# Kernel tuning notes

Hardware: AMD Instinct MI355X
Metric: run time of the kernel (lower is better)

The kernel has to match this reference:

```python
import jax, jax.numpy as jnp
import numpy as np

N = 4096
D = 256
THRESH = 0.04  # default threshold arg of MultiLayerGCN.forward


def setup_inputs() -> dict:
    key = jax.random.key(0)
    ks = jax.random.split(key, 6)
    A = jax.random.normal(ks[0], (N, N), dtype=jnp.float32)
    features = jax.random.normal(ks[1], (N, D), dtype=jnp.float32)
    s = 0.02
    W1 = jax.random.normal(ks[2], (D, D), dtype=jnp.float32) * s
    b1 = jax.random.normal(ks[3], (D,), dtype=jnp.float32) * s
    W2 = jax.random.normal(ks[4], (D, D), dtype=jnp.float32) * s
    b2 = jax.random.normal(ks[5], (D,), dtype=jnp.float32) * s
    return {"A": A, "features": features, "W1": W1, "b1": b1, "W2": W2, "b2": b2}


def _graph_conv(C, out_isqrt, in_isqrt, h, W, b):
    # DGL GraphConv, norm='both': scale src by out_deg^-1/2, aggregate over
    # edges u->v (rst[v] = sum_u C[u,v] * h[u]), scale dst by in_deg^-1/2.
    h = (h * out_isqrt[:, None]) @ W            # [N, out]
    agg = jnp.einsum('uv,ud->vd', C, h)          # C^T @ h, honoring edge direction
    return agg * in_isqrt[:, None] + b


def reference(A, features, W1, b1, W2, b2):
    dt = features.dtype
    mask = (A >= THRESH).astype(dt)
    # add_edges(nodes, nodes) adds self loops on top of surviving diagonal -> counts
    C = mask + jnp.eye(A.shape[0], dtype=dt)
    out_deg = jnp.maximum(C.sum(axis=1), 1.0)    # clamp(min=1) as in DGL
    in_deg = jnp.maximum(C.sum(axis=0), 1.0)
    out_isqrt = jax.lax.rsqrt(out_deg)
    in_isqrt = jax.lax.rsqrt(in_deg)
    h1 = jax.nn.relu(_graph_conv(C, out_isqrt, in_isqrt, features, W1, b1))
    h2 = jax.nn.relu(_graph_conv(C, out_isqrt, in_isqrt, h1, W2, b2))
    return (h1, h2)
```

## Files before the change

kernel.cpp:

```cpp
#include <hip/hip_runtime.h>
#include <stdint.h>

#define NN 4096
#define DD 256
#define TH 0.04f

typedef __attribute__((ext_vector_type(4))) float f32x4;
typedef __attribute__((ext_vector_type(16))) float f32x16;
typedef __attribute__((ext_vector_type(8))) short s16x8;
typedef unsigned short us;

__device__ __forceinline__ us f2bf(float f) {
  union { float f; uint32_t u; } x; x.f = f;
  uint32_t u = x.u;
  return (us)((u + 0x7FFFu + ((u >> 16) & 1u)) >> 16);
}
__device__ __forceinline__ float bf2f(us h) {
  union { uint32_t u; float f; } x; x.u = ((uint32_t)h) << 16;
  return x.f;
}

__device__ __forceinline__ void hw_selfstage(const float* __restrict__ H,
                                             const float* __restrict__ W,
                                             int u0,
                                             us* __restrict__ hWb,
                                             us* __restrict__ hWbP,
                                             char* smem) {
  us (*hs)[264] = reinterpret_cast<us(*)[264]>(smem);
  us (*wt)[34]  = reinterpret_cast<us(*)[34]>(smem + 16 * 264 * 2);
  us (*lt)[260] = reinterpret_cast<us(*)[260]>(smem + 16 * 264 * 2 + 256 * 34 * 2);
  const int t = threadIdx.x;
#pragma unroll
  for (int rep = 0; rep < 4; ++rep) {
    const int flat = rep * 256 + t;
    const int row = flat >> 6, c4 = (flat & 63) * 4;
    f32x4 v = *reinterpret_cast<const f32x4*>(H + (size_t)(u0 + row) * DD + c4);
    uint2 pw;
    pw.x = (uint32_t)f2bf(v[0]) | ((uint32_t)f2bf(v[1]) << 16);
    pw.y = (uint32_t)f2bf(v[2]) | ((uint32_t)f2bf(v[3]) << 16);
    *reinterpret_cast<uint2*>(&hs[row][c4]) = pw;
  }
  const int lane = t & 63, w = t >> 6, l15 = lane & 15, l4 = lane >> 4;
  const f32x4 z = {0.f, 0.f, 0.f, 0.f};
  f32x4 acc[4];
#pragma unroll
  for (int jn = 0; jn < 4; ++jn) acc[jn] = z;
#pragma unroll 1
  for (int ks = 0; ks < 8; ++ks) {
    __syncthreads();
#pragma unroll
    for (int rr = 0; rr < 8; ++rr) {
      const int flat = rr * 256 + t;
      const int k = flat >> 6, d0 = (flat & 63) * 4;
      f32x4 wv = *reinterpret_cast<const f32x4*>(W + (size_t)(ks * 32 + k) * DD + d0);
      wt[d0 + 0][k] = f2bf(wv[0]);
      wt[d0 + 1][k] = f2bf(wv[1]);
      wt[d0 + 2][k] = f2bf(wv[2]);
      wt[d0 + 3][k] = f2bf(wv[3]);
    }
    __syncthreads();
    s16x8 af = *reinterpret_cast<const s16x8*>(&hs[l15][ks * 32 + l4 * 8]);
#pragma unroll
    for (int jn = 0; jn < 4; ++jn) {
      const int dt = w * 4 + jn;
      s16x8 bf = *reinterpret_cast<const s16x8*>(&wt[dt * 16 + l15][l4 * 8]);
      acc[jn] = __builtin_amdgcn_mfma_f32_16x16x32_bf16(af, bf, acc[jn], 0, 0, 0);
    }
  }
#pragma unroll
  for (int jn = 0; jn < 4; ++jn) {
    const int d = w * 64 + jn * 16 + l15;
#pragma unroll
    for (int r = 0; r < 4; ++r) {
      const int ul = l4 * 4 + r;
      us hv = f2bf(acc[jn][r]);
      hWb[(size_t)(u0 + ul) * DD + d] = hv;
      lt[ul][d] = hv;
    }
  }
  __syncthreads();
  const int sg = u0 >> 4;
#pragma unroll
  for (int cc = 0; cc < 2; ++cc) {
    const int c = t * 2 + cc;
    const int dt = c >> 6, lc = c & 63;
    const int ub = (lc >> 5) * 8;
    const int d = dt * 32 + (lc & 31);
    uint4 val;
    val.x = (uint32_t)lt[ub + 0][d] | ((uint32_t)lt[ub + 1][d] << 16);
    val.y = (uint32_t)lt[ub + 2][d] | ((uint32_t)lt[ub + 3][d] << 16);
    val.z = (uint32_t)lt[ub + 4][d] | ((uint32_t)lt[ub + 5][d] << 16);
    val.w = (uint32_t)lt[ub + 6][d] | ((uint32_t)lt[ub + 7][d] << 16);
    *reinterpret_cast<uint4*>(hWbP + ((size_t)dt * 256 + sg) * 512 + lc * 8) = val;
  }
}

__global__ __launch_bounds__(256) void k_scanhw1(const float* __restrict__ A,
                                                 const float* __restrict__ feat,
                                                 const float* __restrict__ W1,
                                                 const float* __restrict__ W2,
                                                 us* __restrict__ bitsT,
                                                 unsigned char* __restrict__ colpart,
                                                 float* __restrict__ oif,
                                                 us* __restrict__ oib,
                                                 us* __restrict__ hWb1,
                                                 us* __restrict__ hWbP1,
                                                 us* __restrict__ W2TbP) {
  __shared__ __align__(16) char smem[34176];
  const int b = blockIdx.x, t = threadIdx.x;
  const int r3 = b % 3;
  if (r3 == 2) {
    hw_selfstage(feat, W1, (b / 3) * 16, hWb1, hWbP1, smem);
    return;
  }
  const int sb = (b / 3) * 2 + r3;
  us* lds16 = reinterpret_cast<us*>(smem);
  const int u0 = sb * 8;
  uint32_t cs[16];
#pragma unroll
  for (int k = 0; k < 16; ++k) cs[k] = 0;
#pragma unroll
  for (int rb = 0; rb < 2; ++rb) {
    f32x4 a[4][4];
#pragma unroll
    for (int r = 0; r < 4; ++r) {
      const f32x4* p = reinterpret_cast<const f32x4*>(A + (size_t)(u0 + rb * 4 + r) * NN + t * 16);
#pragma unroll
      for (int c = 0; c < 4; ++c) a[r][c] = p[c];
    }
#pragma unroll
    for (int r = 0; r < 4; ++r) {
      uint32_t m = 0;
#pragma unroll
      for (int c = 0; c < 4; ++c)
#pragma unroll
        for (int j = 0; j < 4; ++j) m |= (a[r][c][j] >= TH ? 1u : 0u) << (c * 4 + j);
      lds16[t * 8 + rb * 4 + r] = (us)m;
#pragma unroll
      for (int k = 0; k < 16; ++k) cs[k] += (m >> k) & 1u;
    }
  }
  uint4 pk;
  pk.x = cs[0]  | (cs[1]  << 8) | (cs[2]  << 16) | (cs[3]  << 24);
  pk.y = cs[4]  | (cs[5]  << 8) | (cs[6]  << 16) | (cs[7]  << 24);
  pk.z = cs[8]  | (cs[9]  << 8) | (cs[10] << 16) | (cs[11] << 24);
  pk.w = cs[12] | (cs[13] << 8) | (cs[14] << 16) | (cs[15] << 24);
  *reinterpret_cast<uint4*>(colpart + (size_t)sb * 4096 + t * 16) = pk;
  __syncthreads();
  uint4 wv4 = *reinterpret_cast<const uint4*>(&lds16[t * 8]);
  *reinterpret_cast<uint4*>(bitsT + (size_t)t * 4096 + u0) = wv4;
  if (t < 64) {
    const int r = t >> 3, part = t & 7;
    uint32_t s = 0;
#pragma unroll
    for (int wv = part * 32; wv < part * 32 + 32; ++wv)
      s += (uint32_t)__popc((uint32_t)lds16[wv * 8 + r]);
    s += __shfl_down(s, 4, 8);
    s += __shfl_down(s, 2, 8);
    s += __shfl_down(s, 1, 8);
    if (part == 0) {
      float val = rsqrtf((float)(s + 1u));
      oif[u0 + r] = val;
      oib[u0 + r] = f2bf(val);
    }
  }
  if (sb < 16) {
    const int base = sb * 4096 + t * 16;
#pragma unroll
    for (int e = 0; e < 16; ++e) {
      const int idx = base + e;
      const int frag = idx >> 9, pos = idx & 511;
      const int lc = pos >> 3, j = pos & 7;
      const int dt = frag >> 3, ks = frag & 7;
      const int k = ks * 32 + (lc >> 4) * 8 + j;
      const int d = dt * 16 + (lc & 15);
      W2TbP[idx] = f2bf(W2[k * 256 + d]);
    }
  }
}

__global__ __launch_bounds__(256) void k_hw2(const float* __restrict__ H,
                                             const us* __restrict__ WP,
                                             const float* __restrict__ oif,
                                             us* __restrict__ hWb,
                                             us* __restrict__ hWbP) {
  __shared__ us hs[16][264];
  __shared__ us lt[16][260];
  const int t = threadIdx.x;
  const int u0 = blockIdx.x * 16;
#pragma unroll
  for (int rep = 0; rep < 4; ++rep) {
    const int flat = rep * 256 + t;
    const int row = flat >> 6, c4 = (flat & 63) * 4;
    f32x4 v = *reinterpret_cast<const f32x4*>(H + (size_t)(u0 + row) * DD + c4);
    uint2 pw;
    pw.x = (uint32_t)f2bf(v[0]) | ((uint32_t)f2bf(v[1]) << 16);
    pw.y = (uint32_t)f2bf(v[2]) | ((uint32_t)f2bf(v[3]) << 16);
    *reinterpret_cast<uint2*>(&hs[row][c4]) = pw;
  }
  __syncthreads();
  const int lane = t & 63, w = t >> 6, l15 = lane & 15, l4 = lane >> 4;
  const f32x4 z = {0.f, 0.f, 0.f, 0.f};
  f32x4 acc[4];
#pragma unroll
  for (int jn = 0; jn < 4; ++jn) acc[jn] = z;
#pragma unroll
  for (int ks = 0; ks < 8; ++ks) {
    s16x8 af = *reinterpret_cast<const s16x8*>(&hs[l15][ks * 32 + l4 * 8]);
#pragma unroll
    for (int jn = 0; jn < 4; ++jn) {
      const int dt = w * 4 + jn;
      s16x8 bf = *reinterpret_cast<const s16x8*>(WP + ((size_t)dt * 8 + ks) * 512 + lane * 8);
      acc[jn] = __builtin_amdgcn_mfma_f32_16x16x32_bf16(af, bf, acc[jn], 0, 0, 0);
    }
  }
  float oifv[4];
#pragma unroll
  for (int r = 0; r < 4; ++r) oifv[r] = oif[u0 + l4 * 4 + r];
#pragma unroll
  for (int jn = 0; jn < 4; ++jn) {
    const int d = w * 64 + jn * 16 + l15;
#pragma unroll
    for (int r = 0; r < 4; ++r) {
      const int ul = l4 * 4 + r;
      us hv = f2bf(acc[jn][r] * oifv[r]);
      hWb[(size_t)(u0 + ul) * DD + d] = hv;
      lt[ul][d] = hv;
    }
  }
  __syncthreads();
  const int sg = u0 >> 4;
#pragma unroll
  for (int cc = 0; cc < 2; ++cc) {
    const int c = t * 2 + cc;
    const int dt = c >> 6, lc = c & 63;
    const int ub = (lc >> 5) * 8;
    const int d = dt * 32 + (lc & 31);
    uint4 val;
    val.x = (uint32_t)lt[ub + 0][d] | ((uint32_t)lt[ub + 1][d] << 16);
    val.y = (uint32_t)lt[ub + 2][d] | ((uint32_t)lt[ub + 3][d] << 16);
    val.z = (uint32_t)lt[ub + 4][d] | ((uint32_t)lt[ub + 5][d] << 16);
    val.w = (uint32_t)lt[ub + 6][d] | ((uint32_t)lt[ub + 7][d] << 16);
    *reinterpret_cast<uint4*>(hWbP + ((size_t)dt * 256 + sg) * 512 + lc * 8) = val;
  }
}

template <int L1>
__global__ __launch_bounds__(512, 2) void k_spmm(const us* __restrict__ bitsT,
                                                 const us* __restrict__ hWbP,
                                                 const us* __restrict__ hWb,
                                                 const float* __restrict__ oif,
                                                 const us* __restrict__ oib,
                                                 const unsigned char* __restrict__ colpart,
                                                 float* __restrict__ ii_g,
                                                 const float* __restrict__ bias,
                                                 float* __restrict__ dst) {
  __shared__ float lds[4 * 64 * 68];
  __shared__ float ii_s[64];
  const int t = threadIdx.x, bq = blockIdx.x;
  const int lane = t & 63, w = t >> 6;
  const int mi = w & 1, kc = w >> 1;
  const int xcd = bq & 7, jj = bq >> 3;
  const int vt = xcd * 8 + (jj >> 2), dq = jj & 3;
  const int V0 = vt * 64, D0 = dq * 64;

  const int l31 = lane & 31, l5 = lane >> 5;
  const uint32_t sh = lane & 15;
  const int wvl = vt * 4 + mi * 2 + ((lane >> 4) & 1);
  const us* Ab = bitsT + (size_t)wvl * 4096 + kc * 1024 + l5 * 8;
  const us* Ob = oib + kc * 1024 + l5 * 8;
  const us* Bp0 = hWbP + ((size_t)(dq * 2 + 0) * 256 + kc * 64) * 512 + lane * 8;
  const us* Bp1 = hWbP + ((size_t)(dq * 2 + 1) * 256 + kc * 64) * 512 + lane * 8;

  f32x16 acc0, acc1;
#pragma unroll
  for (int q = 0; q < 16; ++q) { acc0[q] = 0.f; acc1[q] = 0.f; }

  uint4 h[4]; s16x8 o[4], p0[4], p1[4];
#pragma unroll
  for (int sl = 0; sl < 4; ++sl) {
    h[sl]  = *reinterpret_cast<const uint4*>(Ab + sl * 16);
    if (L1) o[sl] = *reinterpret_cast<const s16x8*>(Ob + sl * 16);
    p0[sl] = *reinterpret_cast<const s16x8*>(Bp0 + (size_t)sl * 512);
    p1[sl] = *reinterpret_cast<const s16x8*>(Bp1 + (size_t)sl * 512);
  }

#pragma unroll 1
  for (int it = 0; it < 16; ++it) {
#pragma unroll
    for (int sl = 0; sl < 4; ++sl) {
      union { s16x8 v; uint32_t u[4]; } af;
      uint32_t m;
      if (L1) {
        const uint32_t* ou = reinterpret_cast<const uint32_t*>(&o[sl]);
        m = (h[sl].x >> sh) & 0x10001u; af.u[0] = ou[0] & ((m << 16) - m);
        m = (h[sl].y >> sh) & 0x10001u; af.u[1] = ou[1] & ((m << 16) - m);
        m = (h[sl].z >> sh) & 0x10001u; af.u[2] = ou[2] & ((m << 16) - m);
        m = (h[sl].w >> sh) & 0x10001u; af.u[3] = ou[3] & ((m << 16) - m);
      } else {
        m = (h[sl].x >> sh) & 0x10001u; af.u[0] = m * 0x3F80u;
        m = (h[sl].y >> sh) & 0x10001u; af.u[1] = m * 0x3F80u;
        m = (h[sl].z >> sh) & 0x10001u; af.u[2] = m * 0x3F80u;
        m = (h[sl].w >> sh) & 0x10001u; af.u[3] = m * 0x3F80u;
      }
      acc0 = __builtin_amdgcn_mfma_f32_32x32x16_bf16(af.v, p0[sl], acc0, 0, 0, 0);
      acc1 = __builtin_amdgcn_mfma_f32_32x32x16_bf16(af.v, p1[sl], acc1, 0, 0, 0);
      const int ns = (it * 4 + sl + 4) & 63;
      h[sl]  = *reinterpret_cast<const uint4*>(Ab + ns * 16);
      if (L1) o[sl] = *reinterpret_cast<const s16x8*>(Ob + ns * 16);
      p0[sl] = *reinterpret_cast<const s16x8*>(Bp0 + (size_t)ns * 512);
      p1[sl] = *reinterpret_cast<const s16x8*>(Bp1 + (size_t)ns * 512);
    }
  }

  if (L1) {
    uint32_t* sc = reinterpret_cast<uint32_t*>(lds);
    const int v4 = t & 15, c = t >> 4;
    uint32_t s0 = 0, s1 = 0;
#pragma unroll 4
    for (int r = 0; r < 16; ++r) {
      uint32_t x = *reinterpret_cast<const uint32_t*>(colpart + (size_t)(c * 16 + r) * 4096 + V0 + v4 * 4);
      s0 += x & 0x00FF00FFu;
      s1 += (x >> 8) & 0x00FF00FFu;
    }
    sc[(c * 16 + v4) * 2] = s0;
    sc[(c * 16 + v4) * 2 + 1] = s1;
    __syncthreads();
    if (t < 64) {
      const int v4b = t >> 2, sub = t & 3;
      const int reg = sub & 1, hi = sub >> 1;
      uint32_t s = 0;
#pragma unroll
      for (int cc = 0; cc < 32; ++cc)
        s += (sc[(cc * 16 + v4b) * 2 + reg] >> (hi * 16)) & 0xFFFFu;
      float val = rsqrtf((float)(s + 1u));
      ii_s[t] = val;
      ii_g[V0 + t] = val;
    }
    __syncthreads();
  } else {
    if (t < 64) ii_s[t] = ii_g[V0 + t];
  }

  float* buf = lds + (size_t)kc * (64 * 68);
#pragma unroll
  for (int reg = 0; reg < 16; ++reg) {
    const int row = (reg & 3) + 8 * (reg >> 2) + 4 * l5;
    buf[(mi * 32 + row) * 68 + l31] = acc0[reg];
    buf[(mi * 32 + row) * 68 + 32 + l31] = acc1[reg];
  }
  __syncthreads();

  const int vloc = t >> 3, d8 = (t & 7) * 8;
  const int v = V0 + vloc;
  const float* base = lds + vloc * 68 + d8;
  f32x4 s0v = *reinterpret_cast<const f32x4*>(base);
  f32x4 s1v = *reinterpret_cast<const f32x4*>(base + 4);
#pragma unroll
  for (int q = 1; q < 4; ++q) {
    s0v += *reinterpret_cast<const f32x4*>(base + q * (64 * 68));
    s1v += *reinterpret_cast<const f32x4*>(base + q * (64 * 68) + 4);
  }
  union { s16x8 v; us u[8]; } self;
  self.v = *reinterpret_cast<const s16x8*>(hWb + (size_t)v * DD + D0 + d8);
  const float iv = ii_s[vloc];
  const float ov = L1 ? oif[v] : 1.0f;
  const f32x4 bi0 = *reinterpret_cast<const f32x4*>(bias + D0 + d8);
  const f32x4 bi1 = *reinterpret_cast<const f32x4*>(bias + D0 + d8 + 4);
  f32x4 o0, o1;
#pragma unroll
  for (int e = 0; e < 4; ++e) {
    o0[e] = fmaxf((s0v[e] + ov * bf2f(self.u[e])) * iv + bi0[e], 0.f);
    o1[e] = fmaxf((s1v[e] + ov * bf2f(self.u[e + 4])) * iv + bi1[e], 0.f);
  }
  f32x4* po = reinterpret_cast<f32x4*>(dst + (size_t)v * DD + D0 + d8);
  po[0] = o0; po[1] = o1;
}

extern "C" void kernel_launch(void* const* d_in, const int* in_sizes, int n_in,
                              void* d_out, int out_size, void* d_ws, size_t ws_size,
                              hipStream_t stream) {
  const float* A    = (const float*)d_in[0];
  const float* feat = (const float*)d_in[1];
  const float* W1   = (const float*)d_in[2];
  const float* b1   = (const float*)d_in[3];
  const float* W2   = (const float*)d_in[4];
  const float* b2   = (const float*)d_in[5];
  float* out = (float*)d_out;
  char* ws = (char*)d_ws;

  us*            bitsT   = (us*)ws;
  unsigned char* colpart = (unsigned char*)(ws + (2u << 20));
  us*            hWbP1   = (us*)(ws + (4u << 20));
  us*            hWb1    = (us*)(ws + (6u << 20));
  us*            hWbP2   = (us*)(ws + (8u << 20));
  us*            hWb2    = (us*)(ws + (10u << 20));
  us*            W2TbP   = (us*)(ws + (12u << 20));
  float*         oif     = (float*)(ws + (12u << 20) + (1u << 17));
  us*            oib     = (us*)(ws + (12u << 20) + (1u << 17) + (16u << 10));
  float*         ii_g    = (float*)(ws + (12u << 20) + (1u << 17) + (24u << 10));

  k_scanhw1<<<768, 256, 0, stream>>>(A, feat, W1, W2, bitsT, colpart, oif, oib,
                                     hWb1, hWbP1, W2TbP);
  k_spmm<1><<<256, 512, 0, stream>>>(bitsT, hWbP1, hWb1, oif, oib, colpart,
                                     ii_g, b1, out);
  k_hw2<<<256, 256, 0, stream>>>(out, W2TbP, oif, hWb2, hWbP2);
  k_spmm<0><<<256, 512, 0, stream>>>(bitsT, hWbP2, hWb2, oif, oib, colpart,
                                     ii_g, b2, out + (size_t)NN * DD);
}
```

Measured before the change: 70.94 us.

## Fuse layer-1 aggregation with layer-2 feature transform into one kernel

Replaces the layer-1 SpMM plus separate hW2 GEMM kernel with a single kernel in which each block owns 16 destination rows across all 256 feature columns. It aggregates with 16x16x32 MFMAs, computes in-degree norms, applies bias/ReLU, then immediately multiplies by W2 from LDS to emit the layer-2 packed operands. It also folds the out-degree scaling into the layer-2 operand so the second SpMM drops the oif multiply. The hWbP1 packing layout changes to suit the new kernel. This removes one launch and a global round trip of h1, but each block now streams the full bit matrix row and the whole K range with smaller MFMA tiles, which may reduce reuse of the B operand.

```diff
diff --git a/kernel.cpp b/kernel.cpp
--- a/kernel.cpp
+++ b/kernel.cpp
@@ -79,19 +79,20 @@
     }
   }
   __syncthreads();
-  const int sg = u0 >> 4;
-#pragma unroll
-  for (int cc = 0; cc < 2; ++cc) {
-    const int c = t * 2 + cc;
-    const int dt = c >> 6, lc = c & 63;
-    const int ub = (lc >> 5) * 8;
-    const int d = dt * 32 + (lc & 31);
+  const int ks2 = u0 >> 5, half = (u0 >> 4) & 1;
+#pragma unroll
+  for (int e = 0; e < 2; ++e) {
+    const int s = t * 2 + e;
+    const int f = s >> 5, lrel = s & 31;
+    const int l = half * 32 + lrel;
+    const int ub = (lrel >> 4) * 8;
+    const int d = f * 16 + (lrel & 15);
     uint4 val;
     val.x = (uint32_t)lt[ub + 0][d] | ((uint32_t)lt[ub + 1][d] << 16);
     val.y = (uint32_t)lt[ub + 2][d] | ((uint32_t)lt[ub + 3][d] << 16);
     val.z = (uint32_t)lt[ub + 4][d] | ((uint32_t)lt[ub + 5][d] << 16);
     val.w = (uint32_t)lt[ub + 6][d] | ((uint32_t)lt[ub + 7][d] << 16);
-    *reinterpret_cast<uint4*>(hWbP + ((size_t)dt * 256 + sg) * 512 + lc * 8) = val;
+    *reinterpret_cast<uint4*>(hWbP + ((size_t)f * 128 + ks2) * 512 + l * 8) = val;
   }
 }
 
@@ -179,82 +180,155 @@
   }
 }
 
-__global__ __launch_bounds__(256) void k_hw2(const float* __restrict__ H,
-                                             const us* __restrict__ WP,
-                                             const float* __restrict__ oif,
-                                             us* __restrict__ hWb,
-                                             us* __restrict__ hWbP) {
-  __shared__ us hs[16][264];
-  __shared__ us lt[16][260];
-  const int t = threadIdx.x;
-  const int u0 = blockIdx.x * 16;
-#pragma unroll
-  for (int rep = 0; rep < 4; ++rep) {
-    const int flat = rep * 256 + t;
-    const int row = flat >> 6, c4 = (flat & 63) * 4;
-    f32x4 v = *reinterpret_cast<const f32x4*>(H + (size_t)(u0 + row) * DD + c4);
-    uint2 pw;
-    pw.x = (uint32_t)f2bf(v[0]) | ((uint32_t)f2bf(v[1]) << 16);
-    pw.y = (uint32_t)f2bf(v[2]) | ((uint32_t)f2bf(v[3]) << 16);
-    *reinterpret_cast<uint2*>(&hs[row][c4]) = pw;
-  }
-  __syncthreads();
-  const int lane = t & 63, w = t >> 6, l15 = lane & 15, l4 = lane >> 4;
-  const f32x4 z = {0.f, 0.f, 0.f, 0.f};
-  f32x4 acc[4];
-#pragma unroll
-  for (int jn = 0; jn < 4; ++jn) acc[jn] = z;
+__global__ __launch_bounds__(512, 2) void k_l1f(const us* __restrict__ bitsT,
+                                                const us* __restrict__ hWbP1,
+                                                const us* __restrict__ hWb1,
+                                                const float* __restrict__ oif,
+                                                const us* __restrict__ oib,
+                                                const unsigned char* __restrict__ colpart,
+                                                const us* __restrict__ W2TbP,
+                                                float* __restrict__ ii_g,
+                                                const float* __restrict__ b1,
+                                                float* __restrict__ out,
+                                                us* __restrict__ hWb2,
+                                                us* __restrict__ hWbP2) {
+  __shared__ __align__(16) uint32_t sc[128 * 4 * 2];
+  __shared__ us g[16][264];
+  __shared__ us p2l[16][264];
+  __shared__ float ii_s[16];
+  const int t = threadIdx.x, wv = blockIdx.x;
+  const int lane = t & 63, w = t >> 6;
+  const int V0 = wv * 16;
+  const int l15 = lane & 15, l4 = lane >> 4;
+  const uint32_t sh = (uint32_t)l15;
+
+  const us* Ab = bitsT + (size_t)wv * 4096 + l4 * 8;
+  const us* Ob = oib + l4 * 8;
+  const us* Bp0 = hWbP1 + ((size_t)(w * 2 + 0) * 128) * 512 + lane * 8;
+  const us* Bp1 = hWbP1 + ((size_t)(w * 2 + 1) * 128) * 512 + lane * 8;
+
+  f32x4 acc0 = {0.f, 0.f, 0.f, 0.f}, acc1 = {0.f, 0.f, 0.f, 0.f};
+  uint4 h[4]; s16x8 o[4], p0[4], p1[4];
+#pragma unroll
+  for (int sl = 0; sl < 4; ++sl) {
+    h[sl]  = *reinterpret_cast<const uint4*>(Ab + sl * 32);
+    o[sl]  = *reinterpret_cast<const s16x8*>(Ob + sl * 32);
+    p0[sl] = *reinterpret_cast<const s16x8*>(Bp0 + (size_t)sl * 512);
+    p1[sl] = *reinterpret_cast<const s16x8*>(Bp1 + (size_t)sl * 512);
+  }
+#pragma unroll 1
+  for (int it = 0; it < 32; ++it) {
+#pragma unroll
+    for (int sl = 0; sl < 4; ++sl) {
+      union { s16x8 v; uint32_t u[4]; } af;
+      const uint32_t* ou = reinterpret_cast<const uint32_t*>(&o[sl]);
+      uint32_t m;
+      m = (h[sl].x >> sh) & 0x10001u; af.u[0] = ou[0] & ((m << 16) - m);
+      m = (h[sl].y >> sh) & 0x10001u; af.u[1] = ou[1] & ((m << 16) - m);
+      m = (h[sl].z >> sh) & 0x10001u; af.u[2] = ou[2] & ((m << 16) - m);
+      m = (h[sl].w >> sh) & 0x10001u; af.u[3] = ou[3] & ((m << 16) - m);
+      acc0 = __builtin_amdgcn_mfma_f32_16x16x32_bf16(af.v, p0[sl], acc0, 0, 0, 0);
+      acc1 = __builtin_amdgcn_mfma_f32_16x16x32_bf16(af.v, p1[sl], acc1, 0, 0, 0);
+      const int ns = (it * 4 + sl + 4) & 127;
+      h[sl]  = *reinterpret_cast<const uint4*>(Ab + ns * 32);
+      o[sl]  = *reinterpret_cast<const s16x8*>(Ob + ns * 32);
+      p0[sl] = *reinterpret_cast<const s16x8*>(Bp0 + (size_t)ns * 512);
+      p1[sl] = *reinterpret_cast<const s16x8*>(Bp1 + (size_t)ns * 512);
+    }
+  }
+
+  {
+    const int v4 = t & 3, c = t >> 2;
+    uint32_t s0 = 0, s1 = 0;
+#pragma unroll
+    for (int r = 0; r < 4; ++r) {
+      uint32_t x = *reinterpret_cast<const uint32_t*>(colpart + (size_t)(c * 4 + r) * 4096 + V0 + v4 * 4);
+      s0 += x & 0x00FF00FFu;
+      s1 += (x >> 8) & 0x00FF00FFu;
+    }
+    sc[(c * 4 + v4) * 2] = s0;
+    sc[(c * 4 + v4) * 2 + 1] = s1;
+  }
+  __syncthreads();
+  if (t < 16) {
+    const int v4b = t >> 2, sub = t & 3;
+    const int reg = sub & 1, hi = sub >> 1;
+    uint32_t s = 0;
+#pragma unroll 8
+    for (int c2 = 0; c2 < 128; ++c2)
+      s += (sc[(c2 * 4 + v4b) * 2 + reg] >> (hi * 16)) & 0xFFFFu;
+    float val = rsqrtf((float)(s + 1u));
+    ii_s[t] = val;
+    ii_g[V0 + t] = val;
+  }
+  __syncthreads();
+
+  {
+    const int d0 = w * 32 + l15, d1 = d0 + 16;
+    const float bv0 = b1[d0], bv1 = b1[d1];
+#pragma unroll
+    for (int r = 0; r < 4; ++r) {
+      const int vloc = l4 * 4 + r;
+      const int v = V0 + vloc;
+      const float iv = ii_s[vloc];
+      const float ov = oif[v];
+      const float self0 = bf2f(hWb1[(size_t)v * DD + d0]);
+      const float self1 = bf2f(hWb1[(size_t)v * DD + d1]);
+      const float h10 = fmaxf((acc0[r] + ov * self0) * iv + bv0, 0.f);
+      const float h11 = fmaxf((acc1[r] + ov * self1) * iv + bv1, 0.f);
+      out[(size_t)v * DD + d0] = h10;
+      out[(size_t)v * DD + d1] = h11;
+      g[vloc][d0] = f2bf(h10 * ov);
+      g[vloc][d1] = f2bf(h11 * ov);
+    }
+  }
+  __syncthreads();
+
+  f32x4 q0 = {0.f, 0.f, 0.f, 0.f}, q1 = {0.f, 0.f, 0.f, 0.f};
 #pragma unroll
   for (int ks = 0; ks < 8; ++ks) {
-    s16x8 af = *reinterpret_cast<const s16x8*>(&hs[l15][ks * 32 + l4 * 8]);
-#pragma unroll
-    for (int jn = 0; jn < 4; ++jn) {
-      const int dt = w * 4 + jn;
-      s16x8 bf = *reinterpret_cast<const s16x8*>(WP + ((size_t)dt * 8 + ks) * 512 + lane * 8);
-      acc[jn] = __builtin_amdgcn_mfma_f32_16x16x32_bf16(af, bf, acc[jn], 0, 0, 0);
-    }
-  }
-  float oifv[4];
-#pragma unroll
-  for (int r = 0; r < 4; ++r) oifv[r] = oif[u0 + l4 * 4 + r];
-#pragma unroll
-  for (int jn = 0; jn < 4; ++jn) {
-    const int d = w * 64 + jn * 16 + l15;
-#pragma unroll
-    for (int r = 0; r < 4; ++r) {
-      const int ul = l4 * 4 + r;
-      us hv = f2bf(acc[jn][r] * oifv[r]);
-      hWb[(size_t)(u0 + ul) * DD + d] = hv;
-      lt[ul][d] = hv;
-    }
-  }
-  __syncthreads();
-  const int sg = u0 >> 4;
-#pragma unroll
-  for (int cc = 0; cc < 2; ++cc) {
-    const int c = t * 2 + cc;
-    const int dt = c >> 6, lc = c & 63;
+    s16x8 af = *reinterpret_cast<const s16x8*>(&g[l15][ks * 32 + l4 * 8]);
+    s16x8 w0 = *reinterpret_cast<const s16x8*>(W2TbP + ((size_t)(w * 2 + 0) * 8 + ks) * 512 + lane * 8);
+    s16x8 w1 = *reinterpret_cast<const s16x8*>(W2TbP + ((size_t)(w * 2 + 1) * 8 + ks) * 512 + lane * 8);
+    q0 = __builtin_amdgcn_mfma_f32_16x16x32_bf16(af, w0, q0, 0, 0, 0);
+    q1 = __builtin_amdgcn_mfma_f32_16x16x32_bf16(af, w1, q1, 0, 0, 0);
+  }
+#pragma unroll
+  for (int r = 0; r < 4; ++r) {
+    const int vloc = l4 * 4 + r;
+    p2l[vloc][w * 32 + l15] = f2bf(q0[r]);
+    p2l[vloc][w * 32 + 16 + l15] = f2bf(q1[r]);
+  }
+  __syncthreads();
+
+  {
+    const int row = t >> 5, d8 = (t & 31) * 8;
+    uint4 val;
+    val.x = (uint32_t)p2l[row][d8 + 0] | ((uint32_t)p2l[row][d8 + 1] << 16);
+    val.y = (uint32_t)p2l[row][d8 + 2] | ((uint32_t)p2l[row][d8 + 3] << 16);
+    val.z = (uint32_t)p2l[row][d8 + 4] | ((uint32_t)p2l[row][d8 + 5] << 16);
+    val.w = (uint32_t)p2l[row][d8 + 6] | ((uint32_t)p2l[row][d8 + 7] << 16);
+    *reinterpret_cast<uint4*>(hWb2 + (size_t)(V0 + row) * DD + d8) = val;
+  }
+  {
+    const int f = t >> 6, lc = t & 63;
     const int ub = (lc >> 5) * 8;
-    const int d = dt * 32 + (lc & 31);
+    const int d = f * 32 + (lc & 31);
     uint4 val;
-    val.x = (uint32_t)lt[ub + 0][d] | ((uint32_t)lt[ub + 1][d] << 16);
-    val.y = (uint32_t)lt[ub + 2][d] | ((uint32_t)lt[ub + 3][d] << 16);
-    val.z = (uint32_t)lt[ub + 4][d] | ((uint32_t)lt[ub + 5][d] << 16);
-    val.w = (uint32_t)lt[ub + 6][d] | ((uint32_t)lt[ub + 7][d] << 16);
-    *reinterpret_cast<uint4*>(hWbP + ((size_t)dt * 256 + sg) * 512 + lc * 8) = val;
-  }
-}
-
-template <int L1>
-__global__ __launch_bounds__(512, 2) void k_spmm(const us* __restrict__ bitsT,
-                                                 const us* __restrict__ hWbP,
-                                                 const us* __restrict__ hWb,
-                                                 const float* __restrict__ oif,
-                                                 const us* __restrict__ oib,
-                                                 const unsigned char* __restrict__ colpart,
-                                                 float* __restrict__ ii_g,
-                                                 const float* __restrict__ bias,
-                                                 float* __restrict__ dst) {
+    val.x = (uint32_t)p2l[ub + 0][d] | ((uint32_t)p2l[ub + 1][d] << 16);
+    val.y = (uint32_t)p2l[ub + 2][d] | ((uint32_t)p2l[ub + 3][d] << 16);
+    val.z = (uint32_t)p2l[ub + 4][d] | ((uint32_t)p2l[ub + 5][d] << 16);
+    val.w = (uint32_t)p2l[ub + 6][d] | ((uint32_t)p2l[ub + 7][d] << 16);
+    *reinterpret_cast<uint4*>(hWbP2 + ((size_t)f * 256 + wv) * 512 + lc * 8) = val;
+  }
+}
+
+__global__ __launch_bounds__(512, 2) void k_spmm2(const us* __restrict__ bitsT,
+                                                  const us* __restrict__ hWbP,
+                                                  const us* __restrict__ hWb,
+                                                  const float* __restrict__ ii_g,
+                                                  const float* __restrict__ bias,
+                                                  float* __restrict__ dst) {
   __shared__ float lds[4 * 64 * 68];
   __shared__ float ii_s[64];
   const int t = threadIdx.x, bq = blockIdx.x;
@@ -268,7 +342,6 @@
   const uint32_t sh = lane & 15;
   const int wvl = vt * 4 + mi * 2 + ((lane >> 4) & 1);
   const us* Ab = bitsT + (size_t)wvl * 4096 + kc * 1024 + l5 * 8;
-  const us* Ob = oib + kc * 1024 + l5 * 8;
   const us* Bp0 = hWbP + ((size_t)(dq * 2 + 0) * 256 + kc * 64) * 512 + lane * 8;
   const us* Bp1 = hWbP + ((size_t)(dq * 2 + 1) * 256 + kc * 64) * 512 + lane * 8;
 
@@ -276,11 +349,10 @@
 #pragma unroll
   for (int q = 0; q < 16; ++q) { acc0[q] = 0.f; acc1[q] = 0.f; }
 
-  uint4 h[4]; s16x8 o[4], p0[4], p1[4];
+  uint4 h[4]; s16x8 p0[4], p1[4];
 #pragma unroll
   for (int sl = 0; sl < 4; ++sl) {
     h[sl]  = *reinterpret_cast<const uint4*>(Ab + sl * 16);
-    if (L1) o[sl] = *reinterpret_cast<const s16x8*>(Ob + sl * 16);
     p0[sl] = *reinterpret_cast<const s16x8*>(Bp0 + (size_t)sl * 512);
     p1[sl] = *reinterpret_cast<const s16x8*>(Bp1 + (size_t)sl * 512);
   }
@@ -291,56 +363,20 @@
     for (int sl = 0; sl < 4; ++sl) {
       union { s16x8 v; uint32_t u[4]; } af;
       uint32_t m;
-      if (L1) {
-        const uint32_t* ou = reinterpret_cast<const uint32_t*>(&o[sl]);
-        m = (h[sl].x >> sh) & 0x10001u; af.u[0] = ou[0] & ((m << 16) - m);
-        m = (h[sl].y >> sh) & 0x10001u; af.u[1] = ou[1] & ((m << 16) - m);
-        m = (h[sl].z >> sh) & 0x10001u; af.u[2] = ou[2] & ((m << 16) - m);
-        m = (h[sl].w >> sh) & 0x10001u; af.u[3] = ou[3] & ((m << 16) - m);
-      } else {
-        m = (h[sl].x >> sh) & 0x10001u; af.u[0] = m * 0x3F80u;
-        m = (h[sl].y >> sh) & 0x10001u; af.u[1] = m * 0x3F80u;
-        m = (h[sl].z >> sh) & 0x10001u; af.u[2] = m * 0x3F80u;
-        m = (h[sl].w >> sh) & 0x10001u; af.u[3] = m * 0x3F80u;
-      }
+      m = (h[sl].x >> sh) & 0x10001u; af.u[0] = m * 0x3F80u;
+      m = (h[sl].y >> sh) & 0x10001u; af.u[1] = m * 0x3F80u;
+      m = (h[sl].z >> sh) & 0x10001u; af.u[2] = m * 0x3F80u;
+      m = (h[sl].w >> sh) & 0x10001u; af.u[3] = m * 0x3F80u;
       acc0 = __builtin_amdgcn_mfma_f32_32x32x16_bf16(af.v, p0[sl], acc0, 0, 0, 0);
       acc1 = __builtin_amdgcn_mfma_f32_32x32x16_bf16(af.v, p1[sl], acc1, 0, 0, 0);
       const int ns = (it * 4 + sl + 4) & 63;
       h[sl]  = *reinterpret_cast<const uint4*>(Ab + ns * 16);
-      if (L1) o[sl] = *reinterpret_cast<const s16x8*>(Ob + ns * 16);
       p0[sl] = *reinterpret_cast<const s16x8*>(Bp0 + (size_t)ns * 512);
       p1[sl] = *reinterpret_cast<const s16x8*>(Bp1 + (size_t)ns * 512);
     }
   }
 
-  if (L1) {
-    uint32_t* sc = reinterpret_cast<uint32_t*>(lds);
-    const int v4 = t & 15, c = t >> 4;
-    uint32_t s0 = 0, s1 = 0;
-#pragma unroll 4
-    for (int r = 0; r < 16; ++r) {
-      uint32_t x = *reinterpret_cast<const uint32_t*>(colpart + (size_t)(c * 16 + r) * 4096 + V0 + v4 * 4);
-      s0 += x & 0x00FF00FFu;
-      s1 += (x >> 8) & 0x00FF00FFu;
-    }
-    sc[(c * 16 + v4) * 2] = s0;
-    sc[(c * 16 + v4) * 2 + 1] = s1;
-    __syncthreads();
-    if (t < 64) {
-      const int v4b = t >> 2, sub = t & 3;
-      const int reg = sub & 1, hi = sub >> 1;
-      uint32_t s = 0;
-#pragma unroll
-      for (int cc = 0; cc < 32; ++cc)
-        s += (sc[(cc * 16 + v4b) * 2 + reg] >> (hi * 16)) & 0xFFFFu;
-      float val = rsqrtf((float)(s + 1u));
-      ii_s[t] = val;
-      ii_g[V0 + t] = val;
-    }
-    __syncthreads();
-  } else {
-    if (t < 64) ii_s[t] = ii_g[V0 + t];
-  }
+  if (t < 64) ii_s[t] = ii_g[V0 + t];
 
   float* buf = lds + (size_t)kc * (64 * 68);
 #pragma unroll
@@ -364,14 +400,13 @@
   union { s16x8 v; us u[8]; } self;
   self.v = *reinterpret_cast<const s16x8*>(hWb + (size_t)v * DD + D0 + d8);
   const float iv = ii_s[vloc];
-  const float ov = L1 ? oif[v] : 1.0f;
   const f32x4 bi0 = *reinterpret_cast<const f32x4*>(bias + D0 + d8);
   const f32x4 bi1 = *reinterpret_cast<const f32x4*>(bias + D0 + d8 + 4);
   f32x4 o0, o1;
 #pragma unroll
   for (int e = 0; e < 4; ++e) {
-    o0[e] = fmaxf((s0v[e] + ov * bf2f(self.u[e])) * iv + bi0[e], 0.f);
-    o1[e] = fmaxf((s1v[e] + ov * bf2f(self.u[e + 4])) * iv + bi1[e], 0.f);
+    o0[e] = fmaxf((s0v[e] + bf2f(self.u[e])) * iv + bi0[e], 0.f);
+    o1[e] = fmaxf((s1v[e] + bf2f(self.u[e + 4])) * iv + bi1[e], 0.f);
   }
   f32x4* po = reinterpret_cast<f32x4*>(dst + (size_t)v * DD + D0 + d8);
   po[0] = o0; po[1] = o1;
@@ -402,9 +437,8 @@
 
   k_scanhw1<<<768, 256, 0, stream>>>(A, feat, W1, W2, bitsT, colpart, oif, oib,
                                      hWb1, hWbP1, W2TbP);
-  k_spmm<1><<<256, 512, 0, stream>>>(bitsT, hWbP1, hWb1, oif, oib, colpart,
-                                     ii_g, b1, out);
-  k_hw2<<<256, 256, 0, stream>>>(out, W2TbP, oif, hWb2, hWbP2);
-  k_spmm<0><<<256, 512, 0, stream>>>(bitsT, hWbP2, hWb2, oif, oib, colpart,
-                                     ii_g, b2, out + (size_t)NN * DD);
-}
+  k_l1f<<<256, 512, 0, stream>>>(bitsT, hWbP1, hWb1, oif, oib, colpart, W2TbP,
+                                 ii_g, b1, out, hWb2, hWbP2);
+  k_spmm2<<<256, 512, 0, stream>>>(bitsT, hWbP2, hWb2, ii_g, b2,
+                                   out + (size_t)NN * DD);
+}
```

After: 80.64 us. 13.7% more time.
